# Kernel optimization log

Measured on AMD Instinct MI355X. Metric: run time of the kernel, lower is better.

Reference implementation:

```python
import jax, jax.numpy as jnp
import numpy as np

VOCAB, EMB, HID, LABELS, NUM_LAYERS = 32000, 512, 1024, 64, 2
B, S = 32, 512


def setup_inputs() -> dict:
    key = jax.random.key(0)
    ks = jax.random.split(key, 12)
    s_e = 1.0 / np.sqrt(EMB)
    s_h = 1.0 / np.sqrt(HID)
    inp = {
        "tokens": jax.random.randint(ks[0], (B, S), 0, VOCAB),
        "emb": jax.random.normal(ks[1], (VOCAB, EMB), jnp.float32),
        # layer 0: input dim EMB
        "W_ih0": jax.random.uniform(ks[2], (HID, EMB), jnp.float32, -s_h, s_h),
        "W_hh0": jax.random.uniform(ks[3], (HID, HID), jnp.float32, -s_h, s_h),
        "b_ih0": jax.random.uniform(ks[4], (HID,), jnp.float32, -s_h, s_h),
        "b_hh0": jax.random.uniform(ks[5], (HID,), jnp.float32, -s_h, s_h),
        # layer 1: input dim HID
        "W_ih1": jax.random.uniform(ks[6], (HID, HID), jnp.float32, -s_h, s_h),
        "W_hh1": jax.random.uniform(ks[7], (HID, HID), jnp.float32, -s_h, s_h),
        "b_ih1": jax.random.uniform(ks[8], (HID,), jnp.float32, -s_h, s_h),
        "b_hh1": jax.random.uniform(ks[9], (HID,), jnp.float32, -s_h, s_h),
        "W_out": jax.random.uniform(ks[10], (LABELS, HID), jnp.float32, -s_h, s_h),
        "b_out": jax.random.uniform(ks[11], (LABELS,), jnp.float32, -s_h, s_h),
    }
    return inp


def _rnn_layer(x, W_ih, W_hh, b_ih, b_hh):
    # x: [B,S,in] -> h_t = tanh(W_ih x_t + b_ih + W_hh h_{t-1} + b_hh)
    # Precompute input projection for all timesteps (one big GEMM).
    xp = jnp.einsum('bsi,hi->bsh', x, W_ih) + (b_ih + b_hh)  # [B,S,H]
    h0 = jnp.zeros((x.shape[0], W_hh.shape[0]), x.dtype)

    def step(h, xt):
        h = jnp.tanh(xt + h @ W_hh.T)
        return h, h

    _, ys = jax.lax.scan(step, h0, jnp.swapaxes(xp, 0, 1))  # [S,B,H]
    return jnp.swapaxes(ys, 0, 1)  # [B,S,H]


def reference(tokens, emb, W_ih0, W_hh0, b_ih0, b_hh0,
              W_ih1, W_hh1, b_ih1, b_hh1, W_out, b_out):
    x = emb[tokens]  # [B,S,EMB]
    h = _rnn_layer(x, W_ih0, W_hh0, b_ih0, b_hh0)
    h = _rnn_layer(h, W_ih1, W_hh1, b_ih1, b_hh1)
    return jnp.einsum('bsh,lh->bsl', h, W_out) + b_out  # [B,S,LABELS]
```

## Files before the change

### kernel.cpp

```cpp
#include <hip/hip_runtime.h>
#include <math.h>

#define B_    32
#define S_    512
#define EMB_  512
#define HID_  1024
#define LAB_  64
#define M_    (B_ * S_)

#define SLOT_U64   2048
#define LS_STRIDE  (8 * SLOT_U64)
#define EX_TOTAL   (2 * 4 * LS_STRIDE)
#define EPBIT      0x40000000u
#define NANPAT64   0x7FC000007FC00000ULL
#define PAYMASK    0xBFFFFFFFu

typedef unsigned int u32x4 __attribute__((ext_vector_type(4)));

__device__ __forceinline__ void astore64(unsigned long long* p, unsigned long long v) {
    __hip_atomic_store(p, v, __ATOMIC_RELAXED, __HIP_MEMORY_SCOPE_AGENT);
}
__device__ __forceinline__ void apoll2(const unsigned long long* q0,
                                       const unsigned long long* q1,
                                       u32x4& w0, u32x4& w1) {
    asm volatile(
        "global_load_dwordx4 %0, %2, off sc1\n\t"
        "global_load_dwordx4 %1, %3, off sc1\n\t"
        "s_waitcnt vmcnt(0)"
        : "=&v"(w0), "=&v"(w1)
        : "v"(q0), "v"(q1)
        : "memory");
}
__device__ __forceinline__ bool epok4(u32x4 v, unsigned eb) {
    return ((((v[0] ^ eb) | (v[1] ^ eb)) | ((v[2] ^ eb) | (v[3] ^ eb)))
            & EPBIT) == 0;
}
__device__ __forceinline__ float fold16(float* v, int kg) {
#pragma unroll
    for (int st = 0; st < 4; ++st) {
        const int m  = 1 << st;
        const int nh = 8 >> st;
        const bool hi = (kg & m) != 0;
#pragma unroll
        for (int j = 0; j < 8; ++j) {
            if (j < nh) {
                const float a0 = v[2*j], a1 = v[2*j+1];
                const float got = __shfl_xor(hi ? a0 : a1, m, 64);
                v[j] = (hi ? a1 : a0) + got;
            }
        }
    }
    float r = v[0];
    r += __shfl_xor(r, 16, 64);
    r += __shfl_xor(r, 32, 64);
    return r;
}

__global__ __launch_bounds__(256) void gemm_bias(
    const float* __restrict__ A, const int* __restrict__ tokens,
    const float* __restrict__ W, const float* __restrict__ bias,
    const float* __restrict__ bias2, float* __restrict__ C,
    int M, int K, int N)
{
    __shared__ float As[128][17];
    __shared__ float Ws[64][17];

    const int tid = threadIdx.x;
    const int tx  = tid & 15;
    const int ty  = tid >> 4;
    const int n0  = blockIdx.x * 64;
    const int m0  = blockIdx.y * 128;

    const int lr  = tid >> 2;
    const int lk  = (tid & 3) << 2;

    const int ar0 = tokens ? tokens[m0 + lr]      : (m0 + lr);
    const int ar1 = tokens ? tokens[m0 + 64 + lr] : (m0 + 64 + lr);
    const float* __restrict__ arow0 = A + (size_t)ar0 * K;
    const float* __restrict__ arow1 = A + (size_t)ar1 * K;
    const float* __restrict__ wrow  = W + (size_t)(n0 + lr) * K;

    float bs[4];
#pragma unroll
    for (int j = 0; j < 4; ++j) {
        int n = n0 + tx * 4 + j;
        bs[j] = bias[n] + (bias2 ? bias2[n] : 0.0f);
    }

    float acc[8][4] = {};

    for (int k0 = 0; k0 < K; k0 += 16) {
        const float4 a0 = *(const float4*)(arow0 + k0 + lk);
        const float4 a1 = *(const float4*)(arow1 + k0 + lk);
        const float4 wv = *(const float4*)(wrow  + k0 + lk);
        __syncthreads();
        As[lr][lk + 0] = a0.x; As[lr][lk + 1] = a0.y;
        As[lr][lk + 2] = a0.z; As[lr][lk + 3] = a0.w;
        As[64 + lr][lk + 0] = a1.x; As[64 + lr][lk + 1] = a1.y;
        As[64 + lr][lk + 2] = a1.z; As[64 + lr][lk + 3] = a1.w;
        Ws[lr][lk + 0] = wv.x; Ws[lr][lk + 1] = wv.y;
        Ws[lr][lk + 2] = wv.z; Ws[lr][lk + 3] = wv.w;
        __syncthreads();

#pragma unroll
        for (int kk = 0; kk < 16; ++kk) {
            float b[4], a[8];
#pragma unroll
            for (int j = 0; j < 4; ++j) b[j] = Ws[tx * 4 + j][kk];
#pragma unroll
            for (int i = 0; i < 8; ++i) a[i] = As[ty * 8 + i][kk];
#pragma unroll
            for (int i = 0; i < 8; ++i)
#pragma unroll
                for (int j = 0; j < 4; ++j)
                    acc[i][j] += a[i] * b[j];
        }
    }

#pragma unroll
    for (int i = 0; i < 8; ++i) {
        const int m = m0 + ty * 8 + i;
        float4 v;
        v.x = acc[i][0] + bs[0];
        v.y = acc[i][1] + bs[1];
        v.z = acc[i][2] + bs[2];
        v.w = acc[i][3] + bs[3];
        *(float4*)(C + (size_t)m * N + n0 + tx * 4) = v;
    }
}

__global__ __launch_bounds__(256) void fill_poison(unsigned long long* p, int n)
{
    const int i = blockIdx.x * 256 + threadIdx.x;
    if (i < n) p[i] = NANPAT64;
}

__global__ __launch_bounds__(512, 2) void rnn_fused(
    const float* __restrict__ Whh0, const float* __restrict__ Whh1,
    const float* __restrict__ Wih1, const float* __restrict__ b_ih1,
    const float* __restrict__ b_hh1, float* __restrict__ xb,
    unsigned long long* __restrict__ ex)
{
    extern __shared__ float smem[];
    float2* hb = (float2*)smem;

    const int wg  = blockIdx.x;
    const int g   = wg & 7;
    const int s   = wg >> 3;
    const int tid = threadIdx.x;
    const int j8  = tid >> 6;
    const int kg  = tid & 63;
    const int b0  = g * 4;

    float w0[4][16], wx[4][16], wh[4][16];
    {
        const size_t base = (size_t)(s * 32 + j8 * 4) * HID_ + kg;
#pragma unroll
        for (int i = 0; i < 4; ++i)
#pragma unroll
            for (int q = 0; q < 16; ++q) {
                const size_t o = base + (size_t)i * HID_ + (size_t)q * 64;
                w0[i][q] = Whh0[o];
                wx[i][q] = Wih1[o];
                wh[i][q] = Whh1[o];
            }
    }

    const int i4 = (kg >> 2) & 3;
    const int bb = kg & 3;
    const int ok = s * 32 + j8 * 4 + i4;
    float bsum = 0.f;
    if (kg < 16) bsum = b_ih1[ok] + b_hh1[ok];

    float* px0 = xb + ((size_t)(b0 + bb) * S_) * HID_ + ok;
    float* px1 = px0;

    unsigned long long* const exg = ex + (size_t)g * SLOT_U64;
    const int c0 = 2 * tid, c1 = 1024 + 2 * tid;

    for (int r = 0; r <= S_ + 1; ++r) {
        float xpv = 0.f;
        if (kg < 16 && r < S_) xpv = *px0;
        px0 += HID_;

        float2* sA = hb + (size_t)(r % 3) * 2048;
        float2* sP = hb + (size_t)((r + 2) % 3) * 2048;
        float2* s1 = hb + (size_t)(3 + (r & 1)) * 2048;

        if (r == 0) {
#pragma unroll
            for (int k = 0; k < 4; ++k)
                sA[tid + 512 * k] = make_float2(0.f, 0.f);
        }
        if (r == 2) {
#pragma unroll
            for (int k = 0; k < 4; ++k)
                s1[tid + 512 * k] = make_float2(0.f, 0.f);
        }
        {
            unsigned pend = ((r >= 1 && r <= S_) ? 3u : 0u)
                          | ((r >= 3) ? 0xCu : 0u);
            if (pend) {
                const unsigned long long* pl0 =
                    exg + (size_t)((r - 1) & 3) * LS_STRIDE;
                const unsigned long long* pl1 =
                    exg + (size_t)(4 + ((r - 3) & 3)) * LS_STRIDE;
                const unsigned eb0 = ((((unsigned)(r - 1)) >> 2) & 1u) << 30;
                const unsigned eb1 = ((((unsigned)(r - 3)) >> 2) & 1u) << 30;
                u32x4 a0, a1, d0, d1;
                do {
                    if (pend & 3u) {
                        apoll2(pl0 + c0, pl0 + c1, a0, a1);
                        if ((pend & 1u) && epok4(a0, eb0)) {
                            sA[tid]        = make_float2(
                                __uint_as_float(a0[0] & PAYMASK),
                                __uint_as_float(a0[1] & PAYMASK));
                            sA[1024 + tid] = make_float2(
                                __uint_as_float(a0[2] & PAYMASK),
                                __uint_as_float(a0[3] & PAYMASK));
                            pend &= ~1u;
                        }
                        if ((pend & 2u) && epok4(a1, eb0)) {
                            sA[512 + tid]  = make_float2(
                                __uint_as_float(a1[0] & PAYMASK),
                                __uint_as_float(a1[1] & PAYMASK));
                            sA[1536 + tid] = make_float2(
                                __uint_as_float(a1[2] & PAYMASK),
                                __uint_as_float(a1[3] & PAYMASK));
                            pend &= ~2u;
                        }
                    }
                    if (pend & 0xCu) {
                        apoll2(pl1 + c0, pl1 + c1, d0, d1);
                        if ((pend & 4u) && epok4(d0, eb1)) {
                            s1[tid]        = make_float2(
                                __uint_as_float(d0[0] & PAYMASK),
                                __uint_as_float(d0[1] & PAYMASK));
                            s1[1024 + tid] = make_float2(
                                __uint_as_float(d0[2] & PAYMASK),
                                __uint_as_float(d0[3] & PAYMASK));
                            pend &= ~4u;
                        }
                        if ((pend & 8u) && epok4(d1, eb1)) {
                            s1[512 + tid]  = make_float2(
                                __uint_as_float(d1[0] & PAYMASK),
                                __uint_as_float(d1[1] & PAYMASK));
                            s1[1536 + tid] = make_float2(
                                __uint_as_float(d1[2] & PAYMASK),
                                __uint_as_float(d1[3] & PAYMASK));
                            pend &= ~8u;
                        }
                    }
                } while (pend);
            }
        }
        __syncthreads();

        if (r < S_) {
            float v[16] = {};
#pragma unroll
            for (int q = 0; q < 16; ++q) {
                const float2 a0 = sA[q * 64 + kg];
                const float2 a1 = sA[1024 + q * 64 + kg];
#pragma unroll
                for (int i = 0; i < 4; ++i) {
                    const float fa = w0[i][q];
                    v[i*4+0] += fa * a0.x; v[i*4+1] += fa * a0.y;
                    v[i*4+2] += fa * a1.x; v[i*4+3] += fa * a1.y;
                }
            }
            const float r0 = fold16(v, kg);
            float h0 = 0.f;
            if (kg < 16) h0 = tanhf(xpv + r0);
            const float h0p = __shfl_xor(h0, 1, 64);
            if (kg < 16 && (bb & 1) == 0) {
                const unsigned pe = (((unsigned)r >> 2) & 1u) << 30;
                const unsigned long long u =
                    ((unsigned long long)(__float_as_uint(h0p) | pe) << 32) |
                    (unsigned long long)(__float_as_uint(h0) | pe);
                astore64(exg + (size_t)(r & 3) * LS_STRIDE
                             + 2 * ok + (bb >> 1), u);
            }
        }

        if (r >= 2) {
            float v[16] = {};
#pragma unroll
            for (int q = 0; q < 16; ++q) {
                const float2 a0 = sP[q * 64 + kg];
                const float2 a1 = sP[1024 + q * 64 + kg];
                const float2 c0f = s1[q * 64 + kg];
                const float2 c1f = s1[1024 + q * 64 + kg];
#pragma unroll
                for (int i = 0; i < 4; ++i) {
                    const float fb = wx[i][q];
                    v[i*4+0] += fb * a0.x; v[i*4+1] += fb * a0.y;
                    v[i*4+2] += fb * a1.x; v[i*4+3] += fb * a1.y;
                    const float fc = wh[i][q];
                    v[i*4+0] += fc * c0f.x; v[i*4+1] += fc * c0f.y;
                    v[i*4+2] += fc * c1f.x; v[i*4+3] += fc * c1f.y;
                }
            }
            const float r1 = fold16(v, kg);
            float h1 = 0.f;
            if (kg < 16) h1 = tanhf(r1 + bsum);
            const float h1p = __shfl_xor(h1, 1, 64);
            if (kg < 16) *px1 = h1;
            if (kg < 16 && (bb & 1) == 0) {
                const unsigned pe = (((unsigned)(r - 2) >> 2) & 1u) << 30;
                const unsigned long long u =
                    ((unsigned long long)(__float_as_uint(h1p) | pe) << 32) |
                    (unsigned long long)(__float_as_uint(h1) | pe);
                astore64(exg + (size_t)(4 + ((r - 2) & 3)) * LS_STRIDE
                             + 2 * ok + (bb >> 1), u);
            }
            px1 += HID_;
        }
    }
}

extern "C" void kernel_launch(void* const* d_in, const int* in_sizes, int n_in,
                              void* d_out, int out_size, void* d_ws, size_t ws_size,
                              hipStream_t stream)
{
    const int*   tokens = (const int*)  d_in[0];
    const float* emb    = (const float*)d_in[1];
    const float* W_ih0  = (const float*)d_in[2];
    const float* W_hh0  = (const float*)d_in[3];
    const float* b_ih0  = (const float*)d_in[4];
    const float* b_hh0  = (const float*)d_in[5];
    const float* W_ih1  = (const float*)d_in[6];
    const float* W_hh1  = (const float*)d_in[7];
    const float* b_ih1  = (const float*)d_in[8];
    const float* b_hh1  = (const float*)d_in[9];
    const float* W_out  = (const float*)d_in[10];
    const float* b_out  = (const float*)d_in[11];
    float* out = (float*)d_out;

    float* buf = (float*)d_ws;
    unsigned long long* ex = (unsigned long long*)d_out;

    const size_t scan_lds = 98304;
    hipFuncSetAttribute((const void*)rnn_fused,
                        hipFuncAttributeMaxDynamicSharedMemorySize, (int)scan_lds);

    gemm_bias<<<dim3(HID_ / 64, M_ / 128), 256, 0, stream>>>(
        emb, tokens, W_ih0, b_ih0, b_hh0, buf, M_, EMB_, HID_);

    fill_poison<<<EX_TOTAL / 256, 256, 0, stream>>>(ex, EX_TOTAL);

    rnn_fused<<<256, 512, scan_lds, stream>>>(
        W_hh0, W_hh1, W_ih1, b_ih1, b_hh1, buf, ex);

    gemm_bias<<<dim3(LAB_ / 64, M_ / 128), 256, 0, stream>>>(
        buf, nullptr, W_out, b_out, nullptr, out, M_, HID_, LAB_);
}
```

Measured before the change: 3.132 ms.

## Overlap layer-0 state polling with layer-1 compute in persistent RNN loop

Restructures the per-step schedule of the persistent wavefront RNN kernel. Layer-1 inputs are polled first, then the layer-0 hidden-state loads are issued asynchronously and the layer-1 matvec runs while they are in flight. Only after that does the kernel wait on those loads, spin if they are not yet ready, and run the layer-0 step. The aim is to hide cross-block exchange latency on the critical layer-0 recurrence behind layer-1 work. In exchange it adds a second barrier per step and uses hand-written waitcnt/barrier asm.

```diff
diff --git a/kernel.cpp b/kernel.cpp
--- a/kernel.cpp
+++ b/kernel.cpp
@@ -30,6 +30,23 @@
         : "=&v"(w0), "=&v"(w1)
         : "v"(q0), "v"(q1)
         : "memory");
+}
+__device__ __forceinline__ void apoll2_issue(const unsigned long long* q0,
+                                             const unsigned long long* q1,
+                                             u32x4& w0, u32x4& w1) {
+    asm volatile(
+        "global_load_dwordx4 %0, %2, off sc1\n\t"
+        "global_load_dwordx4 %1, %3, off sc1"
+        : "=&v"(w0), "=&v"(w1)
+        : "v"(q0), "v"(q1)
+        : "memory");
+}
+__device__ __forceinline__ void vm_wait() {
+    asm volatile("s_waitcnt vmcnt(0)" ::: "memory");
+    __builtin_amdgcn_sched_barrier(0);
+}
+__device__ __forceinline__ void lds_barrier() {
+    asm volatile("s_waitcnt lgkmcnt(0)\n\ts_barrier" ::: "memory");
 }
 __device__ __forceinline__ bool epok4(u32x4 v, unsigned eb) {
     return ((((v[0] ^ eb) | (v[1] ^ eb)) | ((v[2] ^ eb) | (v[3] ^ eb)))
@@ -187,6 +204,13 @@
         float2* sP = hb + (size_t)((r + 2) % 3) * 2048;
         float2* s1 = hb + (size_t)(3 + (r & 1)) * 2048;
 
+        const unsigned eb0 = ((((unsigned)(r - 1)) >> 2) & 1u) << 30;
+        const unsigned eb1 = ((((unsigned)(r - 3)) >> 2) & 1u) << 30;
+        const unsigned long long* pl0 =
+            exg + (size_t)((r - 1) & 3) * LS_STRIDE;
+        const unsigned long long* pl1 =
+            exg + (size_t)(4 + ((r - 3) & 3)) * LS_STRIDE;
+
         if (r == 0) {
 #pragma unroll
             for (int k = 0; k < 4; ++k)
@@ -197,91 +221,37 @@
             for (int k = 0; k < 4; ++k)
                 s1[tid + 512 * k] = make_float2(0.f, 0.f);
         }
-        {
-            unsigned pend = ((r >= 1 && r <= S_) ? 3u : 0u)
-                          | ((r >= 3) ? 0xCu : 0u);
-            if (pend) {
-                const unsigned long long* pl0 =
-                    exg + (size_t)((r - 1) & 3) * LS_STRIDE;
-                const unsigned long long* pl1 =
-                    exg + (size_t)(4 + ((r - 3) & 3)) * LS_STRIDE;
-                const unsigned eb0 = ((((unsigned)(r - 1)) >> 2) & 1u) << 30;
-                const unsigned eb1 = ((((unsigned)(r - 3)) >> 2) & 1u) << 30;
-                u32x4 a0, a1, d0, d1;
-                do {
-                    if (pend & 3u) {
-                        apoll2(pl0 + c0, pl0 + c1, a0, a1);
-                        if ((pend & 1u) && epok4(a0, eb0)) {
-                            sA[tid]        = make_float2(
-                                __uint_as_float(a0[0] & PAYMASK),
-                                __uint_as_float(a0[1] & PAYMASK));
-                            sA[1024 + tid] = make_float2(
-                                __uint_as_float(a0[2] & PAYMASK),
-                                __uint_as_float(a0[3] & PAYMASK));
-                            pend &= ~1u;
-                        }
-                        if ((pend & 2u) && epok4(a1, eb0)) {
-                            sA[512 + tid]  = make_float2(
-                                __uint_as_float(a1[0] & PAYMASK),
-                                __uint_as_float(a1[1] & PAYMASK));
-                            sA[1536 + tid] = make_float2(
-                                __uint_as_float(a1[2] & PAYMASK),
-                                __uint_as_float(a1[3] & PAYMASK));
-                            pend &= ~2u;
-                        }
-                    }
-                    if (pend & 0xCu) {
-                        apoll2(pl1 + c0, pl1 + c1, d0, d1);
-                        if ((pend & 4u) && epok4(d0, eb1)) {
-                            s1[tid]        = make_float2(
-                                __uint_as_float(d0[0] & PAYMASK),
-                                __uint_as_float(d0[1] & PAYMASK));
-                            s1[1024 + tid] = make_float2(
-                                __uint_as_float(d0[2] & PAYMASK),
-                                __uint_as_float(d0[3] & PAYMASK));
-                            pend &= ~4u;
-                        }
-                        if ((pend & 8u) && epok4(d1, eb1)) {
-                            s1[512 + tid]  = make_float2(
-                                __uint_as_float(d1[0] & PAYMASK),
-                                __uint_as_float(d1[1] & PAYMASK));
-                            s1[1536 + tid] = make_float2(
-                                __uint_as_float(d1[2] & PAYMASK),
-                                __uint_as_float(d1[3] & PAYMASK));
-                            pend &= ~8u;
-                        }
-                    }
-                } while (pend);
-            }
-        }
-        __syncthreads();
-
-        if (r < S_) {
-            float v[16] = {};
-#pragma unroll
-            for (int q = 0; q < 16; ++q) {
-                const float2 a0 = sA[q * 64 + kg];
-                const float2 a1 = sA[1024 + q * 64 + kg];
-#pragma unroll
-                for (int i = 0; i < 4; ++i) {
-                    const float fa = w0[i][q];
-                    v[i*4+0] += fa * a0.x; v[i*4+1] += fa * a0.y;
-                    v[i*4+2] += fa * a1.x; v[i*4+3] += fa * a1.y;
-                }
-            }
-            const float r0 = fold16(v, kg);
-            float h0 = 0.f;
-            if (kg < 16) h0 = tanhf(xpv + r0);
-            const float h0p = __shfl_xor(h0, 1, 64);
-            if (kg < 16 && (bb & 1) == 0) {
-                const unsigned pe = (((unsigned)r >> 2) & 1u) << 30;
-                const unsigned long long u =
-                    ((unsigned long long)(__float_as_uint(h0p) | pe) << 32) |
-                    (unsigned long long)(__float_as_uint(h0) | pe);
-                astore64(exg + (size_t)(r & 3) * LS_STRIDE
-                             + 2 * ok + (bb >> 1), u);
-            }
-        }
+        if (r >= 3) {
+            unsigned pend = 3u;
+            u32x4 w0v, w1v;
+            do {
+                apoll2(pl1 + c0, pl1 + c1, w0v, w1v);
+                if ((pend & 1u) && epok4(w0v, eb1)) {
+                    s1[tid]        = make_float2(
+                        __uint_as_float(w0v[0] & PAYMASK),
+                        __uint_as_float(w0v[1] & PAYMASK));
+                    s1[1024 + tid] = make_float2(
+                        __uint_as_float(w0v[2] & PAYMASK),
+                        __uint_as_float(w0v[3] & PAYMASK));
+                    pend &= ~1u;
+                }
+                if ((pend & 2u) && epok4(w1v, eb1)) {
+                    s1[512 + tid]  = make_float2(
+                        __uint_as_float(w1v[0] & PAYMASK),
+                        __uint_as_float(w1v[1] & PAYMASK));
+                    s1[1536 + tid] = make_float2(
+                        __uint_as_float(w1v[2] & PAYMASK),
+                        __uint_as_float(w1v[3] & PAYMASK));
+                    pend &= ~2u;
+                }
+            } while (pend);
+        }
+
+        u32x4 pa0, pa1;
+        const bool needh0 = (r >= 1 && r <= S_);
+        if (needh0) apoll2_issue(pl0 + c0, pl0 + c1, pa0, pa1);
+
+        lds_barrier();
 
         if (r >= 2) {
             float v[16] = {};
@@ -315,6 +285,80 @@
                              + 2 * ok + (bb >> 1), u);
             }
             px1 += HID_;
+        }
+
+        if (needh0) {
+            vm_wait();
+            unsigned pend = 3u;
+            if (epok4(pa0, eb0)) {
+                sA[tid]        = make_float2(
+                    __uint_as_float(pa0[0] & PAYMASK),
+                    __uint_as_float(pa0[1] & PAYMASK));
+                sA[1024 + tid] = make_float2(
+                    __uint_as_float(pa0[2] & PAYMASK),
+                    __uint_as_float(pa0[3] & PAYMASK));
+                pend &= ~1u;
+            }
+            if (epok4(pa1, eb0)) {
+                sA[512 + tid]  = make_float2(
+                    __uint_as_float(pa1[0] & PAYMASK),
+                    __uint_as_float(pa1[1] & PAYMASK));
+                sA[1536 + tid] = make_float2(
+                    __uint_as_float(pa1[2] & PAYMASK),
+                    __uint_as_float(pa1[3] & PAYMASK));
+                pend &= ~2u;
+            }
+            while (pend) {
+                u32x4 w0v, w1v;
+                apoll2(pl0 + c0, pl0 + c1, w0v, w1v);
+                if ((pend & 1u) && epok4(w0v, eb0)) {
+                    sA[tid]        = make_float2(
+                        __uint_as_float(w0v[0] & PAYMASK),
+                        __uint_as_float(w0v[1] & PAYMASK));
+                    sA[1024 + tid] = make_float2(
+                        __uint_as_float(w0v[2] & PAYMASK),
+                        __uint_as_float(w0v[3] & PAYMASK));
+                    pend &= ~1u;
+                }
+                if ((pend & 2u) && epok4(w1v, eb0)) {
+                    sA[512 + tid]  = make_float2(
+                        __uint_as_float(w1v[0] & PAYMASK),
+                        __uint_as_float(w1v[1] & PAYMASK));
+                    sA[1536 + tid] = make_float2(
+                        __uint_as_float(w1v[2] & PAYMASK),
+                        __uint_as_float(w1v[3] & PAYMASK));
+                    pend &= ~2u;
+                }
+            }
+        }
+
+        lds_barrier();
+
+        if (r < S_) {
+            float v[16] = {};
+#pragma unroll
+            for (int q = 0; q < 16; ++q) {
+                const float2 a0 = sA[q * 64 + kg];
+                const float2 a1 = sA[1024 + q * 64 + kg];
+#pragma unroll
+                for (int i = 0; i < 4; ++i) {
+                    const float fa = w0[i][q];
+                    v[i*4+0] += fa * a0.x; v[i*4+1] += fa * a0.y;
+                    v[i*4+2] += fa * a1.x; v[i*4+3] += fa * a1.y;
+                }
+            }
+            const float r0 = fold16(v, kg);
+            float h0 = 0.f;
+            if (kg < 16) h0 = tanhf(xpv + r0);
+            const float h0p = __shfl_xor(h0, 1, 64);
+            if (kg < 16 && (bb & 1) == 0) {
+                const unsigned pe = (((unsigned)r >> 2) & 1u) << 30;
+                const unsigned long long u =
+                    ((unsigned long long)(__float_as_uint(h0p) | pe) << 32) |
+                    (unsigned long long)(__float_as_uint(h0) | pe);
+                astore64(exg + (size_t)(r & 3) * LS_STRIDE
+                             + 2 * ok + (bb >> 1), u);
+            }
         }
     }
 }
```

Result: slower. 3.316 ms (+5.9%).
